# Optimization experiments

Measured on AMD Instinct MI355X. Metric: run time of the kernel, lower is better.

The kernel has to match this reference:

```python
import jax, jax.numpy as jnp
import numpy as np

D = 64       # d_model (channel)
NHEAD = 8    # heads in nn.MultiheadAttention
PROTO = 16   # proto_size == num_queries
EPS = 1e-5


def _haar_filters():
    L = np.array([1.0, 1.0], np.float32) / np.float32(np.sqrt(2.0))
    H = np.array([-1.0, 1.0], np.float32) / np.float32(np.sqrt(2.0))
    # WavePool: LL, LH, HL, HH Haar filters (2x2, stride 2, depthwise)
    return [jnp.asarray(np.outer(a, b)) for (a, b) in ((L, L), (L, H), (H, L), (H, H))]


def _dw(x, k2d, stride):
    # depthwise conv with the SAME 2D filter per channel; x: [B,C,H,W]
    C = x.shape[1]
    k = jnp.tile(k2d[None, None], (C, 1, 1, 1)).astype(x.dtype)
    return jax.lax.conv_general_dilated(x, k, (stride, stride), 'VALID',
        dimension_numbers=('NCHW', 'OIHW', 'NCHW'), feature_group_count=C)


def _ln(x, g, b):
    m = jnp.mean(x, -1, keepdims=True)
    v = jnp.var(x, -1, keepdims=True)
    return (x - m) * jax.lax.rsqrt(v + EPS) * g + b


def _bn(x, g, b, m, v):
    # eval-mode BatchNorm2d, x: [B,C,H,W]
    sh = (1, -1, 1, 1)
    return (x - m.reshape(sh)) * jax.lax.rsqrt(v.reshape(sh) + EPS) * g.reshape(sh) + b.reshape(sh)


def _mscw(x, lw1, lb1, lw2, lb2, gw1, gb1, gw2, gb2):
    pool = jnp.mean(x, axis=1, keepdims=True)            # [B,1,C]
    loc = jax.nn.relu(x @ lw1.T + lb1) @ lw2.T + lb2
    glo = jax.nn.relu(pool @ gw1.T + gb1) @ gw2.T + gb2
    return jax.nn.sigmoid(loc + glo)


def _mha(q, k, v, w_in, b_in, w_out, b_out):
    # standard nn.MultiheadAttention (batch_first), q:[B,Nq,D], k/v:[B,Nk,D]
    B, Nq, d = q.shape
    dk = d // NHEAD
    qp = q @ w_in[:d].T + b_in[:d]
    kp = k @ w_in[d:2 * d].T + b_in[d:2 * d]
    vp = v @ w_in[2 * d:].T + b_in[2 * d:]
    split = lambda t: t.reshape(t.shape[0], t.shape[1], NHEAD, dk).transpose(0, 2, 1, 3)
    qh, kh, vh = split(qp), split(kp), split(vp)
    scores = jnp.einsum('bhqd,bhkd->bhqk', qh, kh) * (1.0 / np.sqrt(dk))
    attn = jax.nn.softmax(scores, axis=-1)
    o = jnp.einsum('bhqk,bhkd->bhqd', attn, vh).transpose(0, 2, 1, 3).reshape(B, Nq, d)
    return o @ w_out.T + b_out


def reference(tgt, memory, pos, query_pos,
              w_in, b_in, w_out, b_out,
              ln1_g, ln1_b, ln2_g, ln2_b,
              m1_lw1, m1_lb1, m1_lw2, m1_lb2, m1_gw1, m1_gb1, m1_gw2, m1_gb2,
              m2_lw1, m2_lb1, m2_lw2, m2_lb2, m2_gw1, m2_gb1, m2_gw2, m2_gb2,
              dw_w, bn1_g, bn1_b, bn1_m, bn1_v, pw_w, bn2_g, bn2_b, bn2_m, bn2_v,
              mheads_w):
    # CrossAttentionLayer.forward_post -> custom MultiheadAttention.forward
    query = (tgt + query_pos).transpose(1, 0, 2)   # [B,Nq,C]
    key = (memory + pos).transpose(1, 0, 2)        # [B,N1,C]
    value = memory.transpose(1, 0, 2)
    B, N1, C = value.shape
    hw = int(np.sqrt(N1))
    feat = key.transpose(0, 2, 1).reshape(B, C, hw, hw)
    fLL, fLH, fHL, fHH = _haar_filters()
    LL = _dw(feat, fLL, 2)
    LH = _dw(feat, fLH, 2)
    HL = _dw(feat, fHL, 2)
    HH = _dw(feat, fHH, 2)
    high = (HL + LH + HH).reshape(B, C, -1).transpose(0, 2, 1)  # [B,N1/4,C]
    low = LL.reshape(B, C, -1).transpose(0, 2, 1)
    wei = _mscw(high + low, m1_lw1, m1_lb1, m1_lw2, m1_lb2, m1_gw1, m1_gb1, m1_gw2, m1_gb2)
    fre = wei * high + low
    x1 = _mha(query, fre, fre, w_in, b_in, w_out, b_out)
    x1 = _ln(x1 + query, ln1_g, ln1_b)
    # DSConv3x3: depthwise 3x3 + BN + ReLU, then 1x1 + BN + ReLU
    y = jax.lax.conv_general_dilated(feat, dw_w, (1, 1), ((1, 1), (1, 1)),
        dimension_numbers=('NCHW', 'OIHW', 'NCHW'), feature_group_count=C)
    y = jax.nn.relu(_bn(y, bn1_g, bn1_b, bn1_m, bn1_v))
    y = jax.lax.conv_general_dilated(y, pw_w, (1, 1), 'VALID',
        dimension_numbers=('NCHW', 'OIHW', 'NCHW'))
    y = jax.nn.relu(_bn(y, bn2_g, bn2_b, bn2_m, bn2_v))
    featf = y.reshape(B, C, -1).transpose(0, 2, 1)          # [B,N1,C]
    mw = jax.nn.softmax(featf @ mheads_w.T, axis=1)          # softmax over tokens, [B,N1,P]
    protos = jnp.einsum('bnp,bnc->bpc', mw, key)             # [B,P,C]
    attn2 = _mscw(protos + query, m2_lw1, m2_lb1, m2_lw2, m2_lb2, m2_gw1, m2_gb1, m2_gw2, m2_gb2)
    x2 = _ln(query * attn2 + query, ln2_g, ln2_b)
    return (x1 + x2).transpose(1, 0, 2)                      # [Nq,B,C]


def setup_inputs() -> dict:
    key = jax.random.key(0)
    ks = iter(jax.random.split(key, 40))
    B, HW, NQ = 8, 128, PROTO
    N1 = HW * HW
    wn = lambda *s: jax.random.normal(next(ks), s, jnp.float32) * 0.05
    inp = {
        'tgt': jax.random.normal(next(ks), (NQ, B, D), jnp.float32),
        'memory': jax.random.normal(next(ks), (N1, B, D), jnp.float32),
        'pos': jax.random.normal(next(ks), (N1, B, D), jnp.float32),
        'query_pos': jax.random.normal(next(ks), (NQ, B, D), jnp.float32),
        'w_in': wn(3 * D, D), 'b_in': jnp.zeros((3 * D,), jnp.float32),
        'w_out': wn(D, D), 'b_out': jnp.zeros((D,), jnp.float32),
        'ln1_g': jnp.ones((D,), jnp.float32), 'ln1_b': jnp.zeros((D,), jnp.float32),
        'ln2_g': jnp.ones((D,), jnp.float32), 'ln2_b': jnp.zeros((D,), jnp.float32),
        'dw_w': wn(D, 1, 3, 3),
        'bn1_g': jnp.ones((D,), jnp.float32), 'bn1_b': jnp.zeros((D,), jnp.float32),
        'bn1_m': jnp.zeros((D,), jnp.float32), 'bn1_v': jnp.ones((D,), jnp.float32),
        'pw_w': wn(D, D, 1, 1),
        'bn2_g': jnp.ones((D,), jnp.float32), 'bn2_b': jnp.zeros((D,), jnp.float32),
        'bn2_m': jnp.zeros((D,), jnp.float32), 'bn2_v': jnp.ones((D,), jnp.float32),
        'mheads_w': wn(PROTO, D),
    }
    for pfx in ('m1', 'm2'):
        for br in ('l', 'g'):
            inp[f'{pfx}_{br}w1'] = wn(D, D)
            inp[f'{pfx}_{br}b1'] = jnp.zeros((D,), jnp.float32)
            inp[f'{pfx}_{br}w2'] = wn(D, D)
            inp[f'{pfx}_{br}b2'] = jnp.zeros((D,), jnp.float32)
    return inp
```

## Files before the change

kernel.cpp:

```cpp
#include <hip/hip_runtime.h>
#include <math.h>

#define N1 16384
#define N2 4096

#define OFF_KEY   0L
#define OFF_KPH   4194304L
#define OFF_VPH   5242880L
#define OFF_PEXP  6291456L
#define OFF_WB    7340032L
#define OFF_CST   7350784L
#define OFF_POOL  7351552L
#define OFF_PROT  7352064L
#define OFF_ZZ    7360256L
#define OFF_GLO   7360384L
#define OFF_QP    7360896L
#define OFF_QB    7369088L
#define OFF_PART  7377280L

typedef __attribute__((ext_vector_type(8))) short bf16x8;
typedef __attribute__((ext_vector_type(4))) float floatx4;

#define MFMA16(a, b, c) __builtin_amdgcn_mfma_f32_16x16x32_bf16(a, b, c, 0, 0, 0)

__device__ __forceinline__ unsigned short f2bf(float f) {
    union { float f; unsigned u; } v; v.f = f;
    unsigned r = v.u + 0x7fffu + ((v.u >> 16) & 1u);
    return (unsigned short)(r >> 16);
}
__device__ __forceinline__ float bf2f(unsigned short s) {
    union { unsigned u; float f; } v; v.u = ((unsigned)s) << 16;
    return v.f;
}
__device__ __forceinline__ float sigmoidf_(float x) { return 1.f / (1.f + __expf(-x)); }
__device__ __forceinline__ bf16x8 ldg8b(const unsigned short* p) { return *(const bf16x8*)p; }
__device__ __forceinline__ void unpack8(uint4 v, float* f) {
    f[0] = bf2f((unsigned short)(v.x & 0xffff)); f[1] = bf2f((unsigned short)(v.x >> 16));
    f[2] = bf2f((unsigned short)(v.y & 0xffff)); f[3] = bf2f((unsigned short)(v.y >> 16));
    f[4] = bf2f((unsigned short)(v.z & 0xffff)); f[5] = bf2f((unsigned short)(v.z >> 16));
    f[6] = bf2f((unsigned short)(v.w & 0xffff)); f[7] = bf2f((unsigned short)(v.w >> 16));
}

__global__ __launch_bounds__(256) void k_prep(const float* __restrict__ lw1,
                                              const float* __restrict__ lw2,
                                              const float* __restrict__ w_in,
                                              const float* __restrict__ pw,
                                              const float* __restrict__ mh,
                                              const float* __restrict__ dw_w,
                                              const float* __restrict__ bn1_g, const float* __restrict__ bn1_b,
                                              const float* __restrict__ bn1_m, const float* __restrict__ bn1_v,
                                              const float* __restrict__ bn2_g, const float* __restrict__ bn2_b,
                                              const float* __restrict__ bn2_m, const float* __restrict__ bn2_v,
                                              unsigned short* __restrict__ wb,
                                              float* __restrict__ cst) {
    int i = blockIdx.x * 256 + threadIdx.x;
    if (i < 21504) {
        float v;
        if (i < 4096) v = lw1[i];
        else if (i < 8192) v = lw2[i - 4096];
        else if (i < 16384) v = w_in[4096 + (i - 8192)];
        else if (i < 20480) v = pw[i - 16384];
        else v = mh[i - 20480];
        wb[i] = f2bf(v);
    } else if (i < 22272) {
        int j = i - 21504;
        if (j < 576) {
            int k = j >> 6, c = j & 63;
            float s1 = bn1_g[c] * rsqrtf(bn1_v[c] + 1e-5f);
            cst[j] = dw_w[c * 9 + k] * s1;
        } else if (j < 640) {
            int c = j - 576;
            float s1 = bn1_g[c] * rsqrtf(bn1_v[c] + 1e-5f);
            cst[j] = bn1_b[c] - bn1_m[c] * s1;
        } else if (j < 704) {
            int c = j - 640;
            cst[j] = bn2_g[c] * rsqrtf(bn2_v[c] + 1e-5f);
        } else {
            int c = j - 704;
            float s2 = bn2_g[c] * rsqrtf(bn2_v[c] + 1e-5f);
            cst[j] = bn2_b[c] - bn2_m[c] * s2;
        }
    }
}

__global__ __launch_bounds__(256) void k_key(const float* __restrict__ mem,
                                             const float* __restrict__ pos,
                                             unsigned short* __restrict__ key,
                                             float* __restrict__ pool1raw) {
    __shared__ float sh[16][64];
    int tid = threadIdx.x;
    int b = blockIdx.x >> 9;
    int n_base = (blockIdx.x & 511) * 32;
    int c8 = tid & 7, local_n = tid >> 3;
    int n = n_base + local_n;
    long s4 = ((long)n * 8 + b) * 16 + c8 * 2;
    float4 m0 = ((const float4*)mem)[s4], m1 = ((const float4*)mem)[s4 + 1];
    float4 p0 = ((const float4*)pos)[s4], p1 = ((const float4*)pos)[s4 + 1];
    float f[8];
    f[0] = m0.x + p0.x; f[1] = m0.y + p0.y; f[2] = m0.z + p0.z; f[3] = m0.w + p0.w;
    f[4] = m1.x + p1.x; f[5] = m1.y + p1.y; f[6] = m1.z + p1.z; f[7] = m1.w + p1.w;
    uint4 o;
    o.x = (unsigned)f2bf(f[0]) | ((unsigned)f2bf(f[1]) << 16);
    o.y = (unsigned)f2bf(f[2]) | ((unsigned)f2bf(f[3]) << 16);
    o.z = (unsigned)f2bf(f[4]) | ((unsigned)f2bf(f[5]) << 16);
    o.w = (unsigned)f2bf(f[6]) | ((unsigned)f2bf(f[7]) << 16);
    ((uint4*)key)[(long)(b * 16384 + n) * 8 + c8] = o;
    int parity = (n_base >> 7) & 1;
    if (parity) {
        if (local_n & 1) {
            #pragma unroll
            for (int j = 0; j < 8; j++) sh[local_n >> 1][c8 * 8 + j] = f[j];
        }
        __syncthreads();
        if (tid < 64) {
            float s = 0.f;
            #pragma unroll
            for (int k = 0; k < 16; k++) s += sh[k][tid];
            atomicAdd(pool1raw + b * 64 + tid, s);
        }
    }
}

__global__ __launch_bounds__(64) void k_qp_glo(const float* __restrict__ tgt,
                                               const float* __restrict__ qpos,
                                               const float* __restrict__ w_in,
                                               const float* __restrict__ b_in,
                                               const float* __restrict__ pool1raw,
                                               const float* __restrict__ gw1, const float* __restrict__ gb1,
                                               const float* __restrict__ gw2, const float* __restrict__ gb2,
                                               float* __restrict__ qp,
                                               float* __restrict__ queryb,
                                               float* __restrict__ glo1) {
    __shared__ float s0[64], s1v[64];
    int t = threadIdx.x;
    if (blockIdx.x < 128) {
        int b = blockIdx.x >> 4;
        int q = blockIdx.x & 15;
        long src = ((long)q * 8 + b) * 64 + t;
        float v = tgt[src] + qpos[src];
        s0[t] = v;
        queryb[(b * 16 + q) * 64 + t] = v;
        __syncthreads();
        float acc = b_in[t];
        for (int c = 0; c < 64; c++) acc += s0[c] * w_in[t * 64 + c];
        qp[(b * 16 + q) * 64 + t] = acc;
    } else {
        int b = blockIdx.x - 128;
        s0[t] = pool1raw[b * 64 + t] * (2.0f / 4096.0f);
        __syncthreads();
        float h = gb1[t];
        for (int c = 0; c < 64; c++) h += s0[c] * gw1[t * 64 + c];
        s1v[t] = fmaxf(h, 0.f);
        __syncthreads();
        float gl = gb2[t];
        for (int hh = 0; hh < 64; hh++) gl += s1v[hh] * gw2[t * 64 + hh];
        glo1[b * 64 + t] = gl;
    }
}

__global__ __launch_bounds__(256) void k_mscw1(
        const unsigned short* __restrict__ keyb, const float* __restrict__ glo1,
        const float* __restrict__ lb1, const float* __restrict__ lb2,
        const float* __restrict__ b_in, const unsigned short* __restrict__ wb,
        unsigned short* __restrict__ kph, unsigned short* __restrict__ vph) {
    __shared__ __align__(16) short stage[256 * 72];
    __shared__ __align__(16) short hbuf[64 * 72];
    __shared__ __align__(16) short wbuf[64 * 72];
    int tid = threadIdx.x;
    int w = tid >> 6, l = tid & 63;
    int b = blockIdx.x >> 6, tile = blockIdx.x & 63;
    int m0 = w * 16, trow = l & 15, oct = l >> 4;
    const unsigned short* src = keyb + ((long)b * 16384 + tile * 256) * 64;
    #pragma unroll
    for (int k = 0; k < 8; k++) {
        int u = k * 256 + tid;
        int p = u >> 3, o = u & 7;
        uint4 v = *(const uint4*)(src + (long)u * 8);
        *(uint4*)(stage + p * 72 + o * 8) = v;
    }
    __syncthreads();
    int j = m0 + trow;
    float x[16], S[16];
    bf16x8 ax[2];
    #pragma unroll
    for (int half = 0; half < 2; half++) {
        int o = oct + half * 4;
        uint4 fa4 = *(const uint4*)(stage + (2 * j) * 72 + o * 8);
        uint4 fb4 = *(const uint4*)(stage + (2 * j + 1) * 72 + o * 8);
        uint4 fc4 = *(const uint4*)(stage + (128 + 2 * j) * 72 + o * 8);
        uint4 fd4 = *(const uint4*)(stage + (129 + 2 * j) * 72 + o * 8);
        float A[8], B[8], C[8], D[8];
        unpack8(fa4, A); unpack8(fb4, B); unpack8(fc4, C); unpack8(fd4, D);
        #pragma unroll
        for (int jj = 0; jj < 8; jj++) {
            float xd = 2.f * D[jj];
            x[half * 8 + jj] = xd;
            S[half * 8 + jj] = 0.5f * (A[jj] + B[jj] + C[jj] + D[jj]);
            ax[half][jj] = (short)f2bf(xd);
        }
    }
    const unsigned short* w1b = wb;
    const unsigned short* w2b = wb + 4096;
    const unsigned short* wkb = wb + 8192;
    const unsigned short* wvb = wb + 12288;
    #pragma unroll
    for (int t4 = 0; t4 < 4; t4++) {
        int n = t4 * 16 + trow;
        float bias = lb1[n];
        floatx4 acc = {bias, bias, bias, bias};
        acc = MFMA16(ax[0], ldg8b(w1b + n * 64 + oct * 8), acc);
        acc = MFMA16(ax[1], ldg8b(w1b + n * 64 + 32 + oct * 8), acc);
        #pragma unroll
        for (int r = 0; r < 4; r++)
            hbuf[(m0 + oct * 4 + r) * 72 + n] = (short)f2bf(fmaxf(acc[r], 0.f));
    }
    __syncthreads();
    {
        bf16x8 ah0 = *(const bf16x8*)(hbuf + (m0 + trow) * 72 + oct * 8);
        bf16x8 ah1 = *(const bf16x8*)(hbuf + (m0 + trow) * 72 + 32 + oct * 8);
        const float* gl = glo1 + b * 64;
        #pragma unroll
        for (int t4 = 0; t4 < 4; t4++) {
            int n = t4 * 16 + trow;
            float bias = lb2[n];
            floatx4 acc = {bias, bias, bias, bias};
            acc = MFMA16(ah0, ldg8b(w2b + n * 64 + oct * 8), acc);
            acc = MFMA16(ah1, ldg8b(w2b + n * 64 + 32 + oct * 8), acc);
            float g = gl[n];
            #pragma unroll
            for (int r = 0; r < 4; r++)
                wbuf[(m0 + oct * 4 + r) * 72 + n] = (short)f2bf(sigmoidf_(acc[r] + g));
        }
    }
    __syncthreads();
    bf16x8 af0, af1;
    {
        bf16x8 w0 = *(const bf16x8*)(wbuf + (m0 + trow) * 72 + oct * 8);
        bf16x8 w1v = *(const bf16x8*)(wbuf + (m0 + trow) * 72 + 32 + oct * 8);
        #pragma unroll
        for (int jj = 0; jj < 8; jj++) {
            float we0 = bf2f((unsigned short)w0[jj]);
            float we1 = bf2f((unsigned short)w1v[jj]);
            af0[jj] = (short)f2bf(we0 * x[jj] + (1.f - we0) * S[jj]);
            af1[jj] = (short)f2bf(we1 * x[8 + jj] + (1.f - we1) * S[8 + jj]);
        }
    }
    __syncthreads();
    short* kbuf = hbuf; short* vbuf = wbuf;
    #pragma unroll
    for (int t4 = 0; t4 < 4; t4++) {
        int ko = t4 * 16 + trow;
        float bk = b_in[64 + ko], bv = b_in[128 + ko];
        floatx4 ak = {bk, bk, bk, bk};
        floatx4 av = {bv, bv, bv, bv};
        ak = MFMA16(af0, ldg8b(wkb + ko * 64 + oct * 8), ak);
        ak = MFMA16(af1, ldg8b(wkb + ko * 64 + 32 + oct * 8), ak);
        av = MFMA16(af0, ldg8b(wvb + ko * 64 + oct * 8), av);
        av = MFMA16(af1, ldg8b(wvb + ko * 64 + 32 + oct * 8), av);
        #pragma unroll
        for (int r = 0; r < 4; r++) {
            int row = m0 + oct * 4 + r;
            kbuf[row * 72 + ko] = (short)f2bf(ak[r]);
            vbuf[row * 72 + ko] = (short)f2bf(av[r]);
        }
    }
    __syncthreads();
    for (int u = tid; u < 512; u += 256) {
        int h = u >> 6, tok = u & 63;
        uint4 kk = *(const uint4*)(kbuf + tok * 72 + h * 8);
        uint4 vv = *(const uint4*)(vbuf + tok * 72 + h * 8);
        long du = (long)(b * 8 + h) * 4096 + tile * 64 + tok;
        ((uint4*)kph)[du] = kk;
        ((uint4*)vph)[du] = vv;
    }
}

__global__ __launch_bounds__(512) void k_dsconv(
        const unsigned short* __restrict__ keyb,
        const unsigned short* __restrict__ wb,
        const float* __restrict__ cst,
        unsigned short* __restrict__ pexp, float* __restrict__ Z) {
    __shared__ __align__(16) short stage[3 * 128 * 72];
    __shared__ __align__(16) short pbuf[16 * 136];
    __shared__ float cbuf[768];
    __shared__ float zred[8][16];
    int tid = threadIdx.x;
    int w = tid >> 6, l = tid & 63;
    int b = blockIdx.x >> 7, h = blockIdx.x & 127;
    int p0 = w * 16, pr = l & 15, oct = l >> 4;
    for (int k = tid; k < 768; k += 512) cbuf[k] = cst[k];
    const unsigned short* kb = keyb + (long)b * 1048576;
    #pragma unroll
    for (int r = 0; r < 3; r++) {
        int row = h - 1 + r;
        if ((unsigned)row < 128u) {
            const unsigned short* src = kb + (long)row * 8192;
            #pragma unroll
            for (int k = 0; k < 4; k++) {
                int u = k * 512 + tid;
                int p = u >> 3, o = u & 7;
                uint4 v = *(const uint4*)(src + (long)u * 8);
                *(uint4*)(stage + (r * 128 + p) * 72 + o * 8) = v;
            }
        } else {
            uint4 zz = {0u, 0u, 0u, 0u};
            #pragma unroll
            for (int k = 0; k < 4; k++) {
                int u = k * 512 + tid;
                int p = u >> 3, o = u & 7;
                *(uint4*)(stage + (r * 128 + p) * 72 + o * 8) = zz;
            }
        }
    }
    __syncthreads();
    float accf[2][8];
    #pragma unroll
    for (int half = 0; half < 2; half++)
        #pragma unroll
        for (int jj = 0; jj < 8; jj++) accf[half][jj] = 0.f;
    #pragma unroll
    for (int r = 0; r < 3; r++) {
        #pragma unroll
        for (int kk = 0; kk < 3; kk++) {
            int col = p0 + pr - 1 + kk;
            if ((unsigned)col < 128u) {
                #pragma unroll
                for (int half = 0; half < 2; half++) {
                    int o = oct + half * 4;
                    uint4 d4 = *(const uint4*)(stage + (r * 128 + col) * 72 + o * 8);
                    float f[8]; unpack8(d4, f);
                    float4 wa = *(const float4*)(cbuf + (r * 3 + kk) * 64 + o * 8);
                    float4 wc = *(const float4*)(cbuf + (r * 3 + kk) * 64 + o * 8 + 4);
                    accf[half][0] += f[0] * wa.x; accf[half][1] += f[1] * wa.y;
                    accf[half][2] += f[2] * wa.z; accf[half][3] += f[3] * wa.w;
                    accf[half][4] += f[4] * wc.x; accf[half][5] += f[5] * wc.y;
                    accf[half][6] += f[6] * wc.z; accf[half][7] += f[7] * wc.w;
                }
            }
        }
    }
    bf16x8 af[2];
    #pragma unroll
    for (int half = 0; half < 2; half++) {
        int o = oct + half * 4;
        float4 oa = *(const float4*)(cbuf + 576 + o * 8);
        float4 ob = *(const float4*)(cbuf + 576 + o * 8 + 4);
        af[half][0] = (short)f2bf(fmaxf(accf[half][0] + oa.x, 0.f));
        af[half][1] = (short)f2bf(fmaxf(accf[half][1] + oa.y, 0.f));
        af[half][2] = (short)f2bf(fmaxf(accf[half][2] + oa.z, 0.f));
        af[half][3] = (short)f2bf(fmaxf(accf[half][3] + oa.w, 0.f));
        af[half][4] = (short)f2bf(fmaxf(accf[half][4] + ob.x, 0.f));
        af[half][5] = (short)f2bf(fmaxf(accf[half][5] + ob.y, 0.f));
        af[half][6] = (short)f2bf(fmaxf(accf[half][6] + ob.z, 0.f));
        af[half][7] = (short)f2bf(fmaxf(accf[half][7] + ob.w, 0.f));
    }
    __syncthreads();
    short* y2buf = stage;
    const unsigned short* pwb = wb + 16384;
    #pragma unroll
    for (int t4 = 0; t4 < 4; t4++) {
        int n = t4 * 16 + pr;
        floatx4 acc = {0.f, 0.f, 0.f, 0.f};
        acc = MFMA16(af[0], ldg8b(pwb + n * 64 + oct * 8), acc);
        acc = MFMA16(af[1], ldg8b(pwb + n * 64 + 32 + oct * 8), acc);
        float s2 = cbuf[640 + n], o2 = cbuf[704 + n];
        #pragma unroll
        for (int r = 0; r < 4; r++)
            y2buf[(p0 + oct * 4 + r) * 72 + n] = (short)f2bf(fmaxf(acc[r] * s2 + o2, 0.f));
    }
    __syncthreads();
    {
        const unsigned short* mhb = wb + 20480;
        bf16x8 a0 = *(const bf16x8*)(y2buf + (p0 + pr) * 72 + oct * 8);
        bf16x8 a1 = *(const bf16x8*)(y2buf + (p0 + pr) * 72 + 32 + oct * 8);
        floatx4 lg = {0.f, 0.f, 0.f, 0.f};
        lg = MFMA16(a0, ldg8b(mhb + pr * 64 + oct * 8), lg);
        lg = MFMA16(a1, ldg8b(mhb + pr * 64 + 32 + oct * 8), lg);
        float zs = 0.f;
        #pragma unroll
        for (int r = 0; r < 4; r++) {
            float e = __expf(lg[r]);
            zs += e;
            pbuf[pr * 136 + p0 + oct * 4 + r] = (short)f2bf(e);
        }
        zs += __shfl_xor(zs, 16);
        zs += __shfl_xor(zs, 32);
        if (l < 16) zred[w][l] = zs;
    }
    __syncthreads();
    if (tid < 256) {
        int p = tid >> 4, ch = tid & 15;
        uint4 o = *(const uint4*)(pbuf + p * 136 + ch * 8);
        ((uint4*)pexp)[((long)(b * 16 + p) * 16384 + h * 128 + ch * 8) >> 3] = o;
    }
    if (tid < 16) {
        float zt = 0.f;
        #pragma unroll
        for (int ww = 0; ww < 8; ww++) zt += zred[ww][tid];
        atomicAdd(Z + b * 16 + tid, zt);
    }
}

__global__ __launch_bounds__(256) void k_protos(const unsigned short* __restrict__ pexp,
                                                const unsigned short* __restrict__ keyb,
                                                float* __restrict__ protos) {
    __shared__ __align__(16) short ldsT[64 * 264];
    int tid = threadIdx.x;
    int b = blockIdx.x >> 6, ch = blockIdx.x & 63;
    long nbase = (long)b * 16384 + ch * 256;
    #pragma unroll
    for (int k = 0; k < 8; k++) {
        int u = k * 256 + tid;
        int n = u >> 3, o = u & 7;
        uint4 v = *(const uint4*)(keyb + (nbase + n) * 64 + o * 8);
        ldsT[(o * 8 + 0) * 264 + n] = (short)(v.x & 0xffff);
        ldsT[(o * 8 + 1) * 264 + n] = (short)(v.x >> 16);
        ldsT[(o * 8 + 2) * 264 + n] = (short)(v.y & 0xffff);
        ldsT[(o * 8 + 3) * 264 + n] = (short)(v.y >> 16);
        ldsT[(o * 8 + 4) * 264 + n] = (short)(v.z & 0xffff);
        ldsT[(o * 8 + 5) * 264 + n] = (short)(v.z >> 16);
        ldsT[(o * 8 + 6) * 264 + n] = (short)(v.w & 0xffff);
        ldsT[(o * 8 + 7) * 264 + n] = (short)(v.w >> 16);
    }
    __syncthreads();
    int w = tid >> 6, l = tid & 63;
    int col = l & 15, oct = l >> 4;
    const unsigned short* pb = pexp + ((long)b * 16 + col) * 16384 + ch * 256;
    floatx4 acc = {0.f, 0.f, 0.f, 0.f};
    #pragma unroll
    for (int s = 0; s < 8; s++) {
        bf16x8 A = *(const bf16x8*)(pb + s * 32 + oct * 8);
        bf16x8 B = *(const bf16x8*)(ldsT + (w * 16 + col) * 264 + s * 32 + oct * 8);
        acc = MFMA16(A, B, acc);
    }
    #pragma unroll
    for (int r = 0; r < 4; r++)
        atomicAdd(protos + (b * 16 + oct * 4 + r) * 64 + w * 16 + col, acc[r]);
}

__global__ __launch_bounds__(256) void k_mha(const float* __restrict__ qp,
                                             const unsigned short* __restrict__ kph,
                                             const unsigned short* __restrict__ vph,
                                             float* __restrict__ part) {
    int bh = blockIdx.x >> 3, seg = blockIdx.x & 7;
    int b = bh >> 3, hh = bh & 7;
    int tid = threadIdx.x;
    int q = tid >> 4, sub = tid & 15;
    const float* qv = qp + (long)(b * 16 + q) * 64 + hh * 8;
    float4 q0 = ((const float4*)qv)[0];
    float4 q1 = ((const float4*)qv)[1];
    const uint4* K4 = (const uint4*)kph + (long)bh * 4096;
    const uint4* V4 = (const uint4*)vph + (long)bh * 4096;
    const float scale = 0.35355339059327373f;
    float m = -1e30f, lsum = 0.f;
    float acc[8];
    #pragma unroll
    for (int d = 0; d < 8; d++) acc[d] = 0.f;
    for (int i = 0; i < 32; i++) {
        int n = seg * 512 + i * 16 + sub;
        float k8[8]; unpack8(K4[n], k8);
        float s = q0.x * k8[0] + q0.y * k8[1] + q0.z * k8[2] + q0.w * k8[3]
                + q1.x * k8[4] + q1.y * k8[5] + q1.z * k8[6] + q1.w * k8[7];
        s *= scale;
        float nm = fmaxf(m, s);
        float corr = __expf(m - nm);
        float wgt = __expf(s - nm);
        lsum = lsum * corr + wgt;
        float v8[8]; unpack8(V4[n], v8);
        #pragma unroll
        for (int d = 0; d < 8; d++) acc[d] = acc[d] * corr + wgt * v8[d];
        m = nm;
    }
    #pragma unroll
    for (int off = 1; off < 16; off <<= 1) {
        float om = __shfl_xor(m, off);
        float ol = __shfl_xor(lsum, off);
        float oa[8];
        #pragma unroll
        for (int d = 0; d < 8; d++) oa[d] = __shfl_xor(acc[d], off);
        float nm = fmaxf(m, om);
        float c1 = __expf(m - nm), c2 = __expf(om - nm);
        lsum = lsum * c1 + ol * c2;
        #pragma unroll
        for (int d = 0; d < 8; d++) acc[d] = acc[d] * c1 + oa[d] * c2;
        m = nm;
    }
    if (sub == 0) {
        float* P = part + ((long)(bh * 16 + q) * 8 + seg) * 12;
        P[0] = m; P[1] = lsum;
        #pragma unroll
        for (int d = 0; d < 8; d++) P[2 + d] = acc[d];
    }
}

__global__ __launch_bounds__(1024) void k_final(
        const float* __restrict__ queryb, const float* __restrict__ protos,
        const float* __restrict__ Z, const float* __restrict__ part,
        const float* __restrict__ w_out, const float* __restrict__ b_out,
        const float* __restrict__ ln1_g, const float* __restrict__ ln1_b,
        const float* __restrict__ ln2_g, const float* __restrict__ ln2_b,
        const float* __restrict__ lw1, const float* __restrict__ lb1,
        const float* __restrict__ lw2, const float* __restrict__ lb2,
        const float* __restrict__ gw1, const float* __restrict__ gb1,
        const float* __restrict__ gw2, const float* __restrict__ gb2,
        float* __restrict__ out) {
    int b = blockIdx.x;
    int t = threadIdx.x >> 6;
    int c = threadIdx.x & 63;
    __shared__ float xs[16][64], hid[16][64], os[16][64];
    __shared__ float pool[64], hidg[64], glo[64];
    float q = queryb[(long)(b * 16 + t) * 64 + c];
    float rz = 1.f / Z[b * 16 + t];
    float xin = protos[(long)(b * 16 + t) * 64 + c] * rz + q;
    xs[t][c] = xin;
    {
        int hh = c >> 3, d = c & 7;
        const float* P = part + ((long)((b * 8 + hh) * 16 + t) * 8) * 12;
        float mm = -1e30f, ll = 0.f, aa = 0.f;
        #pragma unroll
        for (int s = 0; s < 8; s++) {
            float pm = P[s * 12], pl2 = P[s * 12 + 1], pa = P[s * 12 + 2 + d];
            float nm = fmaxf(mm, pm);
            float c1 = __expf(mm - nm), c2 = __expf(pm - nm);
            aa = aa * c1 + pa * c2;
            ll = ll * c1 + pl2 * c2;
            mm = nm;
        }
        os[t][c] = aa / ll;
    }
    __syncthreads();
    if (threadIdx.x < 64) {
        float s = 0.f;
        for (int tt = 0; tt < 16; tt++) s += xs[tt][threadIdx.x];
        pool[threadIdx.x] = s * (1.f / 16.f);
    }
    __syncthreads();
    if (threadIdx.x < 64) {
        int hh = threadIdx.x;
        float a = gb1[hh];
        for (int cc = 0; cc < 64; cc++) a += pool[cc] * gw1[hh * 64 + cc];
        hidg[hh] = fmaxf(a, 0.f);
    }
    __syncthreads();
    if (threadIdx.x < 64) {
        int ccc = threadIdx.x;
        float a = gb2[ccc];
        for (int hh = 0; hh < 64; hh++) a += hidg[hh] * gw2[ccc * 64 + hh];
        glo[ccc] = a;
    }
    float a = lb1[c];
    for (int cc = 0; cc < 64; cc++) a += xs[t][cc] * lw1[c * 64 + cc];
    hid[t][c] = fmaxf(a, 0.f);
    __syncthreads();
    float loc = lb2[c];
    for (int hh = 0; hh < 64; hh++) loc += hid[t][hh] * lw2[c * 64 + hh];
    float attn2 = sigmoidf_(loc + glo[c]);
    float x2p = q * attn2 + q;
    float mu = x2p;
    for (int off = 32; off; off >>= 1) mu += __shfl_down(mu, off);
    mu = __shfl(mu, 0) * (1.f / 64.f);
    float d0 = x2p - mu;
    float vv = d0 * d0;
    for (int off = 32; off; off >>= 1) vv += __shfl_down(vv, off);
    vv = __shfl(vv, 0) * (1.f / 64.f);
    float x2 = d0 * rsqrtf(vv + 1e-5f) * ln2_g[c] + ln2_b[c];
    float x1p = b_out[c];
    for (int k = 0; k < 64; k++) x1p += os[t][k] * w_out[c * 64 + k];
    x1p += q;
    float mu1 = x1p;
    for (int off = 32; off; off >>= 1) mu1 += __shfl_down(mu1, off);
    mu1 = __shfl(mu1, 0) * (1.f / 64.f);
    float d1 = x1p - mu1;
    float v1 = d1 * d1;
    for (int off = 32; off; off >>= 1) v1 += __shfl_down(v1, off);
    v1 = __shfl(v1, 0) * (1.f / 64.f);
    float x1 = d1 * rsqrtf(v1 + 1e-5f) * ln1_g[c] + ln1_b[c];
    out[((long)t * 8 + b) * 64 + c] = x1 + x2;
}

extern "C" void kernel_launch(void* const* d_in, const int* in_sizes, int n_in,
                              void* d_out, int out_size, void* d_ws, size_t ws_size,
                              hipStream_t stream) {
    const float* tgt       = (const float*)d_in[0];
    const float* memory    = (const float*)d_in[1];
    const float* pos       = (const float*)d_in[2];
    const float* query_pos = (const float*)d_in[3];
    const float* w_in      = (const float*)d_in[4];
    const float* b_in      = (const float*)d_in[5];
    const float* w_out     = (const float*)d_in[6];
    const float* b_out     = (const float*)d_in[7];
    const float* ln1_g     = (const float*)d_in[8];
    const float* ln1_b     = (const float*)d_in[9];
    const float* ln2_g     = (const float*)d_in[10];
    const float* ln2_b     = (const float*)d_in[11];
    const float* dw_w      = (const float*)d_in[12];
    const float* bn1_g     = (const float*)d_in[13];
    const float* bn1_b     = (const float*)d_in[14];
    const float* bn1_m     = (const float*)d_in[15];
    const float* bn1_v     = (const float*)d_in[16];
    const float* pw_w      = (const float*)d_in[17];
    const float* bn2_g     = (const float*)d_in[18];
    const float* bn2_b     = (const float*)d_in[19];
    const float* bn2_m     = (const float*)d_in[20];
    const float* bn2_v     = (const float*)d_in[21];
    const float* mheads    = (const float*)d_in[22];
    const float* m1_lw1 = (const float*)d_in[23];
    const float* m1_lb1 = (const float*)d_in[24];
    const float* m1_lw2 = (const float*)d_in[25];
    const float* m1_lb2 = (const float*)d_in[26];
    const float* m1_gw1 = (const float*)d_in[27];
    const float* m1_gb1 = (const float*)d_in[28];
    const float* m1_gw2 = (const float*)d_in[29];
    const float* m1_gb2 = (const float*)d_in[30];
    const float* m2_lw1 = (const float*)d_in[31];
    const float* m2_lb1 = (const float*)d_in[32];
    const float* m2_lw2 = (const float*)d_in[33];
    const float* m2_lb2 = (const float*)d_in[34];
    const float* m2_gw1 = (const float*)d_in[35];
    const float* m2_gb1 = (const float*)d_in[36];
    const float* m2_gw2 = (const float*)d_in[37];
    const float* m2_gb2 = (const float*)d_in[38];

    float* ws = (float*)d_ws;
    float* out = (float*)d_out;
    unsigned short* keyb = (unsigned short*)(ws + OFF_KEY);
    unsigned short* kph  = (unsigned short*)(ws + OFF_KPH);
    unsigned short* vph  = (unsigned short*)(ws + OFF_VPH);
    unsigned short* pexp = (unsigned short*)(ws + OFF_PEXP);
    unsigned short* wb   = (unsigned short*)(ws + OFF_WB);

    hipMemsetAsync(ws + OFF_POOL, 0, 8832 * sizeof(float), stream);

    k_prep<<<88, 256, 0, stream>>>(m1_lw1, m1_lw2, w_in, pw_w, mheads, dw_w,
                                   bn1_g, bn1_b, bn1_m, bn1_v,
                                   bn2_g, bn2_b, bn2_m, bn2_v,
                                   wb, ws + OFF_CST);
    k_key<<<4096, 256, 0, stream>>>(memory, pos, keyb, ws + OFF_POOL);
    k_qp_glo<<<136, 64, 0, stream>>>(tgt, query_pos, w_in, b_in, ws + OFF_POOL,
                                     m1_gw1, m1_gb1, m1_gw2, m1_gb2,
                                     ws + OFF_QP, ws + OFF_QB, ws + OFF_GLO);
    k_mscw1<<<512, 256, 0, stream>>>(keyb, ws + OFF_GLO, m1_lb1, m1_lb2, b_in, wb, kph, vph);
    k_dsconv<<<1024, 512, 0, stream>>>(keyb, wb, ws + OFF_CST, pexp, ws + OFF_ZZ);
    k_protos<<<512, 256, 0, stream>>>(pexp, keyb, ws + OFF_PROT);
    k_mha<<<512, 256, 0, stream>>>(ws + OFF_QP, kph, vph, ws + OFF_PART);
    k_final<<<8, 1024, 0, stream>>>(ws + OFF_QB, ws + OFF_PROT, ws + OFF_ZZ, ws + OFF_PART,
                                    w_out, b_out, ln1_g, ln1_b, ln2_g, ln2_b,
                                    m2_lw1, m2_lb1, m2_lw2, m2_lb2,
                                    m2_gw1, m2_gb1, m2_gw2, m2_gb2,
                                    out);
}
```

Baseline: 267.4 us.

## Fuse prototype GEMM into dsconv, fold query projection into prep, drop pexp buffer

The prototype-weighted key reduction moves into k_dsconv. Each block now transposes its key tile in LDS and runs an MFMA against the softmax buffer, then adds the result into protos atomically. This removes the large bf16 pexp intermediate buffer and the separate k_protos kernel, and with them a write and re-read of several MB. The query projection moves into k_prep and the global-branch MLP is recomputed per block inside k_mscw1, which removes the k_qp_glo launch. Small weight matrices are pre-transposed in k_prep so the per-thread loops in k_final read coalesced memory. The cost is redundant global-MLP work in every k_mscw1 block and more atomic traffic from k_dsconv.

Result: faster. 247.7 us (-7.3%).

```diff
diff --git a/kernel.cpp b/kernel.cpp
--- a/kernel.cpp
+++ b/kernel.cpp
@@ -7,16 +7,14 @@
 #define OFF_KEY   0L
 #define OFF_KPH   4194304L
 #define OFF_VPH   5242880L
-#define OFF_PEXP  6291456L
-#define OFF_WB    7340032L
-#define OFF_CST   7350784L
-#define OFF_POOL  7351552L
-#define OFF_PROT  7352064L
-#define OFF_ZZ    7360256L
-#define OFF_GLO   7360384L
-#define OFF_QP    7360896L
-#define OFF_QB    7369088L
-#define OFF_PART  7377280L
+#define OFF_WB    6291456L
+#define OFF_CST   6302208L
+#define OFF_POOL  6331648L
+#define OFF_PROT  6332160L
+#define OFF_ZZ    6340352L
+#define OFF_QP    6340480L
+#define OFF_QB    6348672L
+#define OFF_PART  6356864L
 
 typedef __attribute__((ext_vector_type(8))) short bf16x8;
 typedef __attribute__((ext_vector_type(4))) float floatx4;
@@ -41,8 +39,8 @@
     f[6] = bf2f((unsigned short)(v.w & 0xffff)); f[7] = bf2f((unsigned short)(v.w >> 16));
 }
 
-__global__ __launch_bounds__(256) void k_prep(const float* __restrict__ lw1,
-                                              const float* __restrict__ lw2,
+__global__ __launch_bounds__(256) void k_prep(const float* __restrict__ m1lw1,
+                                              const float* __restrict__ m1lw2,
                                               const float* __restrict__ w_in,
                                               const float* __restrict__ pw,
                                               const float* __restrict__ mh,
@@ -51,35 +49,73 @@
                                               const float* __restrict__ bn1_m, const float* __restrict__ bn1_v,
                                               const float* __restrict__ bn2_g, const float* __restrict__ bn2_b,
                                               const float* __restrict__ bn2_m, const float* __restrict__ bn2_v,
+                                              const float* __restrict__ m1gw1, const float* __restrict__ m1gw2,
+                                              const float* __restrict__ m2gw1, const float* __restrict__ m2gw2,
+                                              const float* __restrict__ m2lw1, const float* __restrict__ m2lw2,
+                                              const float* __restrict__ w_out,
+                                              const float* __restrict__ tgt, const float* __restrict__ qpos,
+                                              const float* __restrict__ b_in,
                                               unsigned short* __restrict__ wb,
-                                              float* __restrict__ cst) {
-    int i = blockIdx.x * 256 + threadIdx.x;
-    if (i < 21504) {
+                                              float* __restrict__ cst,
+                                              float* __restrict__ qp, float* __restrict__ queryb) {
+    int blk = blockIdx.x, tid = threadIdx.x;
+    if (blk < 84) {
+        int i = blk * 256 + tid;
         float v;
-        if (i < 4096) v = lw1[i];
-        else if (i < 8192) v = lw2[i - 4096];
+        if (i < 4096) v = m1lw1[i];
+        else if (i < 8192) v = m1lw2[i - 4096];
         else if (i < 16384) v = w_in[4096 + (i - 8192)];
         else if (i < 20480) v = pw[i - 16384];
         else v = mh[i - 20480];
         wb[i] = f2bf(v);
-    } else if (i < 22272) {
-        int j = i - 21504;
+    } else if (blk < 199) {
+        int j = (blk - 84) * 256 + tid;
+        float v;
         if (j < 576) {
             int k = j >> 6, c = j & 63;
             float s1 = bn1_g[c] * rsqrtf(bn1_v[c] + 1e-5f);
-            cst[j] = dw_w[c * 9 + k] * s1;
+            v = dw_w[c * 9 + k] * s1;
         } else if (j < 640) {
             int c = j - 576;
             float s1 = bn1_g[c] * rsqrtf(bn1_v[c] + 1e-5f);
-            cst[j] = bn1_b[c] - bn1_m[c] * s1;
+            v = bn1_b[c] - bn1_m[c] * s1;
         } else if (j < 704) {
             int c = j - 640;
-            cst[j] = bn2_g[c] * rsqrtf(bn2_v[c] + 1e-5f);
-        } else {
+            v = bn2_g[c] * rsqrtf(bn2_v[c] + 1e-5f);
+        } else if (j < 768) {
             int c = j - 704;
             float s2 = bn2_g[c] * rsqrtf(bn2_v[c] + 1e-5f);
-            cst[j] = bn2_b[c] - bn2_m[c] * s2;
-        }
+            v = bn2_b[c] - bn2_m[c] * s2;
+        } else {
+            int jj = j - 768;
+            int m = jj >> 12, idx = jj & 4095;
+            int sidx = (idx & 63) * 64 + (idx >> 6);
+            const float* src;
+            switch (m) {
+                case 0: src = m1gw1; break;
+                case 1: src = m1gw2; break;
+                case 2: src = m2gw1; break;
+                case 3: src = m2gw2; break;
+                case 4: src = m2lw1; break;
+                case 5: src = m2lw2; break;
+                default: src = w_out; break;
+            }
+            v = src[sidx];
+        }
+        cst[j] = v;
+    } else {
+        __shared__ float qv[4][64];
+        int g = tid >> 6, lane = tid & 63;
+        int u = (blk - 199) * 4 + g;
+        int b = u >> 4, q = u & 15;
+        long src = ((long)q * 8 + b) * 64 + lane;
+        float v = tgt[src] + qpos[src];
+        qv[g][lane] = v;
+        queryb[(b * 16 + q) * 64 + lane] = v;
+        __syncthreads();
+        float acc = b_in[lane];
+        for (int cc = 0; cc < 64; cc++) acc += qv[g][cc] * w_in[lane * 64 + cc];
+        qp[(b * 16 + q) * 64 + lane] = acc;
     }
 }
 
@@ -121,55 +157,24 @@
     }
 }
 
-__global__ __launch_bounds__(64) void k_qp_glo(const float* __restrict__ tgt,
-                                               const float* __restrict__ qpos,
-                                               const float* __restrict__ w_in,
-                                               const float* __restrict__ b_in,
-                                               const float* __restrict__ pool1raw,
-                                               const float* __restrict__ gw1, const float* __restrict__ gb1,
-                                               const float* __restrict__ gw2, const float* __restrict__ gb2,
-                                               float* __restrict__ qp,
-                                               float* __restrict__ queryb,
-                                               float* __restrict__ glo1) {
-    __shared__ float s0[64], s1v[64];
-    int t = threadIdx.x;
-    if (blockIdx.x < 128) {
-        int b = blockIdx.x >> 4;
-        int q = blockIdx.x & 15;
-        long src = ((long)q * 8 + b) * 64 + t;
-        float v = tgt[src] + qpos[src];
-        s0[t] = v;
-        queryb[(b * 16 + q) * 64 + t] = v;
-        __syncthreads();
-        float acc = b_in[t];
-        for (int c = 0; c < 64; c++) acc += s0[c] * w_in[t * 64 + c];
-        qp[(b * 16 + q) * 64 + t] = acc;
-    } else {
-        int b = blockIdx.x - 128;
-        s0[t] = pool1raw[b * 64 + t] * (2.0f / 4096.0f);
-        __syncthreads();
-        float h = gb1[t];
-        for (int c = 0; c < 64; c++) h += s0[c] * gw1[t * 64 + c];
-        s1v[t] = fmaxf(h, 0.f);
-        __syncthreads();
-        float gl = gb2[t];
-        for (int hh = 0; hh < 64; hh++) gl += s1v[hh] * gw2[t * 64 + hh];
-        glo1[b * 64 + t] = gl;
-    }
-}
-
 __global__ __launch_bounds__(256) void k_mscw1(
-        const unsigned short* __restrict__ keyb, const float* __restrict__ glo1,
+        const unsigned short* __restrict__ keyb, const float* __restrict__ pool1raw,
         const float* __restrict__ lb1, const float* __restrict__ lb2,
+        const float* __restrict__ gb1, const float* __restrict__ gb2,
         const float* __restrict__ b_in, const unsigned short* __restrict__ wb,
+        const float* __restrict__ cst,
         unsigned short* __restrict__ kph, unsigned short* __restrict__ vph) {
     __shared__ __align__(16) short stage[256 * 72];
     __shared__ __align__(16) short hbuf[64 * 72];
     __shared__ __align__(16) short wbuf[64 * 72];
+    __shared__ float parr[64], gtmp[64], gbuf[64];
     int tid = threadIdx.x;
     int w = tid >> 6, l = tid & 63;
     int b = blockIdx.x >> 6, tile = blockIdx.x & 63;
     int m0 = w * 16, trow = l & 15, oct = l >> 4;
+    const float* gw1T = cst + 768;
+    const float* gw2T = cst + 4864;
+    if (tid < 64) parr[tid] = pool1raw[b * 64 + tid] * (2.0f / 4096.0f);
     const unsigned short* src = keyb + ((long)b * 16384 + tile * 256) * 64;
     #pragma unroll
     for (int k = 0; k < 8; k++) {
@@ -179,6 +184,11 @@
         *(uint4*)(stage + p * 72 + o * 8) = v;
     }
     __syncthreads();
+    if (tid < 64) {
+        float a = gb1[tid];
+        for (int cc = 0; cc < 64; cc++) a += parr[cc] * gw1T[cc * 64 + tid];
+        gtmp[tid] = fmaxf(a, 0.f);
+    }
     int j = m0 + trow;
     float x[16], S[16];
     bf16x8 ax[2];
@@ -215,10 +225,15 @@
             hbuf[(m0 + oct * 4 + r) * 72 + n] = (short)f2bf(fmaxf(acc[r], 0.f));
     }
     __syncthreads();
+    if (tid < 64) {
+        float g = gb2[tid];
+        for (int hh = 0; hh < 64; hh++) g += gtmp[hh] * gw2T[hh * 64 + tid];
+        gbuf[tid] = g;
+    }
+    __syncthreads();
     {
         bf16x8 ah0 = *(const bf16x8*)(hbuf + (m0 + trow) * 72 + oct * 8);
         bf16x8 ah1 = *(const bf16x8*)(hbuf + (m0 + trow) * 72 + 32 + oct * 8);
-        const float* gl = glo1 + b * 64;
         #pragma unroll
         for (int t4 = 0; t4 < 4; t4++) {
             int n = t4 * 16 + trow;
@@ -226,7 +241,7 @@
             floatx4 acc = {bias, bias, bias, bias};
             acc = MFMA16(ah0, ldg8b(w2b + n * 64 + oct * 8), acc);
             acc = MFMA16(ah1, ldg8b(w2b + n * 64 + 32 + oct * 8), acc);
-            float g = gl[n];
+            float g = gbuf[n];
             #pragma unroll
             for (int r = 0; r < 4; r++)
                 wbuf[(m0 + oct * 4 + r) * 72 + n] = (short)f2bf(sigmoidf_(acc[r] + g));
@@ -279,7 +294,7 @@
         const unsigned short* __restrict__ keyb,
         const unsigned short* __restrict__ wb,
         const float* __restrict__ cst,
-        unsigned short* __restrict__ pexp, float* __restrict__ Z) {
+        float* __restrict__ protos, float* __restrict__ Z) {
     __shared__ __align__(16) short stage[3 * 128 * 72];
     __shared__ __align__(16) short pbuf[16 * 136];
     __shared__ float cbuf[768];
@@ -356,17 +371,35 @@
     }
     __syncthreads();
     short* y2buf = stage;
-    const unsigned short* pwb = wb + 16384;
-    #pragma unroll
-    for (int t4 = 0; t4 < 4; t4++) {
-        int n = t4 * 16 + pr;
-        floatx4 acc = {0.f, 0.f, 0.f, 0.f};
-        acc = MFMA16(af[0], ldg8b(pwb + n * 64 + oct * 8), acc);
-        acc = MFMA16(af[1], ldg8b(pwb + n * 64 + 32 + oct * 8), acc);
-        float s2 = cbuf[640 + n], o2 = cbuf[704 + n];
-        #pragma unroll
-        for (int r = 0; r < 4; r++)
-            y2buf[(p0 + oct * 4 + r) * 72 + n] = (short)f2bf(fmaxf(acc[r] * s2 + o2, 0.f));
+    short* KT = stage + 18432;
+    {
+        const unsigned short* pwb = wb + 16384;
+        #pragma unroll
+        for (int t4 = 0; t4 < 4; t4++) {
+            int n = t4 * 16 + pr;
+            floatx4 acc = {0.f, 0.f, 0.f, 0.f};
+            acc = MFMA16(af[0], ldg8b(pwb + n * 64 + oct * 8), acc);
+            acc = MFMA16(af[1], ldg8b(pwb + n * 64 + 32 + oct * 8), acc);
+            float s2 = cbuf[640 + n], o2 = cbuf[704 + n];
+            #pragma unroll
+            for (int r = 0; r < 4; r++)
+                y2buf[(p0 + oct * 4 + r) * 72 + n] = (short)f2bf(fmaxf(acc[r] * s2 + o2, 0.f));
+        }
+        #pragma unroll
+        for (int k = 0; k < 2; k++) {
+            int u = k * 512 + tid;
+            int n = u >> 3, o = u & 7;
+            uint4 v = *(const uint4*)(stage + (128 + n) * 72 + o * 8);
+            int nx = n ^ (o << 3);
+            KT[(o * 8 + 0) * 136 + nx] = (short)(v.x & 0xffff);
+            KT[(o * 8 + 1) * 136 + nx] = (short)(v.x >> 16);
+            KT[(o * 8 + 2) * 136 + nx] = (short)(v.y & 0xffff);
+            KT[(o * 8 + 3) * 136 + nx] = (short)(v.y >> 16);
+            KT[(o * 8 + 4) * 136 + nx] = (short)(v.z & 0xffff);
+            KT[(o * 8 + 5) * 136 + nx] = (short)(v.z >> 16);
+            KT[(o * 8 + 6) * 136 + nx] = (short)(v.w & 0xffff);
+            KT[(o * 8 + 7) * 136 + nx] = (short)(v.w >> 16);
+        }
     }
     __syncthreads();
     {
@@ -388,10 +421,20 @@
         if (l < 16) zred[w][l] = zs;
     }
     __syncthreads();
-    if (tid < 256) {
-        int p = tid >> 4, ch = tid & 15;
-        uint4 o = *(const uint4*)(pbuf + p * 136 + ch * 8);
-        ((uint4*)pexp)[((long)(b * 16 + p) * 16384 + h * 128 + ch * 8) >> 3] = o;
+    if (w < 4) {
+        int ct = w;
+        int c = ct * 16 + pr;
+        int xrc = ((c >> 3) & 7) << 3;
+        floatx4 acc = {0.f, 0.f, 0.f, 0.f};
+        #pragma unroll
+        for (int s = 0; s < 4; s++) {
+            bf16x8 A = *(const bf16x8*)(pbuf + pr * 136 + s * 32 + oct * 8);
+            bf16x8 B = *(const bf16x8*)(KT + c * 136 + ((s * 32 + oct * 8) ^ xrc));
+            acc = MFMA16(A, B, acc);
+        }
+        #pragma unroll
+        for (int r = 0; r < 4; r++)
+            atomicAdd(protos + (b * 16 + oct * 4 + r) * 64 + c, acc[r]);
     }
     if (tid < 16) {
         float zt = 0.f;
@@ -399,43 +442,6 @@
         for (int ww = 0; ww < 8; ww++) zt += zred[ww][tid];
         atomicAdd(Z + b * 16 + tid, zt);
     }
-}
-
-__global__ __launch_bounds__(256) void k_protos(const unsigned short* __restrict__ pexp,
-                                                const unsigned short* __restrict__ keyb,
-                                                float* __restrict__ protos) {
-    __shared__ __align__(16) short ldsT[64 * 264];
-    int tid = threadIdx.x;
-    int b = blockIdx.x >> 6, ch = blockIdx.x & 63;
-    long nbase = (long)b * 16384 + ch * 256;
-    #pragma unroll
-    for (int k = 0; k < 8; k++) {
-        int u = k * 256 + tid;
-        int n = u >> 3, o = u & 7;
-        uint4 v = *(const uint4*)(keyb + (nbase + n) * 64 + o * 8);
-        ldsT[(o * 8 + 0) * 264 + n] = (short)(v.x & 0xffff);
-        ldsT[(o * 8 + 1) * 264 + n] = (short)(v.x >> 16);
-        ldsT[(o * 8 + 2) * 264 + n] = (short)(v.y & 0xffff);
-        ldsT[(o * 8 + 3) * 264 + n] = (short)(v.y >> 16);
-        ldsT[(o * 8 + 4) * 264 + n] = (short)(v.z & 0xffff);
-        ldsT[(o * 8 + 5) * 264 + n] = (short)(v.z >> 16);
-        ldsT[(o * 8 + 6) * 264 + n] = (short)(v.w & 0xffff);
-        ldsT[(o * 8 + 7) * 264 + n] = (short)(v.w >> 16);
-    }
-    __syncthreads();
-    int w = tid >> 6, l = tid & 63;
-    int col = l & 15, oct = l >> 4;
-    const unsigned short* pb = pexp + ((long)b * 16 + col) * 16384 + ch * 256;
-    floatx4 acc = {0.f, 0.f, 0.f, 0.f};
-    #pragma unroll
-    for (int s = 0; s < 8; s++) {
-        bf16x8 A = *(const bf16x8*)(pb + s * 32 + oct * 8);
-        bf16x8 B = *(const bf16x8*)(ldsT + (w * 16 + col) * 264 + s * 32 + oct * 8);
-        acc = MFMA16(A, B, acc);
-    }
-    #pragma unroll
-    for (int r = 0; r < 4; r++)
-        atomicAdd(protos + (b * 16 + oct * 4 + r) * 64 + w * 16 + col, acc[r]);
 }
 
 __global__ __launch_bounds__(256) void k_mha(const float* __restrict__ qp,
@@ -496,14 +502,18 @@
 __global__ __launch_bounds__(1024) void k_final(
         const float* __restrict__ queryb, const float* __restrict__ protos,
         const float* __restrict__ Z, const float* __restrict__ part,
-        const float* __restrict__ w_out, const float* __restrict__ b_out,
+        const float* __restrict__ cst,
+        const float* __restrict__ b_out,
         const float* __restrict__ ln1_g, const float* __restrict__ ln1_b,
         const float* __restrict__ ln2_g, const float* __restrict__ ln2_b,
-        const float* __restrict__ lw1, const float* __restrict__ lb1,
-        const float* __restrict__ lw2, const float* __restrict__ lb2,
-        const float* __restrict__ gw1, const float* __restrict__ gb1,
-        const float* __restrict__ gw2, const float* __restrict__ gb2,
+        const float* __restrict__ lb1, const float* __restrict__ lb2,
+        const float* __restrict__ gb1, const float* __restrict__ gb2,
         float* __restrict__ out) {
+    const float* gw1T = cst + 8960;
+    const float* gw2T = cst + 13056;
+    const float* lw1T = cst + 17152;
+    const float* lw2T = cst + 21248;
+    const float* woT  = cst + 25344;
     int b = blockIdx.x;
     int t = threadIdx.x >> 6;
     int c = threadIdx.x & 63;
@@ -538,22 +548,22 @@
     if (threadIdx.x < 64) {
         int hh = threadIdx.x;
         float a = gb1[hh];
-        for (int cc = 0; cc < 64; cc++) a += pool[cc] * gw1[hh * 64 + cc];
+        for (int cc = 0; cc < 64; cc++) a += pool[cc] * gw1T[cc * 64 + hh];
         hidg[hh] = fmaxf(a, 0.f);
     }
     __syncthreads();
     if (threadIdx.x < 64) {
         int ccc = threadIdx.x;
         float a = gb2[ccc];
-        for (int hh = 0; hh < 64; hh++) a += hidg[hh] * gw2[ccc * 64 + hh];
+        for (int hh = 0; hh < 64; hh++) a += hidg[hh] * gw2T[hh * 64 + ccc];
         glo[ccc] = a;
     }
     float a = lb1[c];
-    for (int cc = 0; cc < 64; cc++) a += xs[t][cc] * lw1[c * 64 + cc];
+    for (int cc = 0; cc < 64; cc++) a += xs[t][cc] * lw1T[cc * 64 + c];
     hid[t][c] = fmaxf(a, 0.f);
     __syncthreads();
     float loc = lb2[c];
-    for (int hh = 0; hh < 64; hh++) loc += hid[t][hh] * lw2[c * 64 + hh];
+    for (int hh = 0; hh < 64; hh++) loc += hid[t][hh] * lw2T[hh * 64 + c];
     float attn2 = sigmoidf_(loc + glo[c]);
     float x2p = q * attn2 + q;
     float mu = x2p;
@@ -565,7 +575,7 @@
     vv = __shfl(vv, 0) * (1.f / 64.f);
     float x2 = d0 * rsqrtf(vv + 1e-5f) * ln2_g[c] + ln2_b[c];
     float x1p = b_out[c];
-    for (int k = 0; k < 64; k++) x1p += os[t][k] * w_out[c * 64 + k];
+    for (int k = 0; k < 64; k++) x1p += os[t][k] * woT[k * 64 + c];
     x1p += q;
     float mu1 = x1p;
     for (int off = 32; off; off >>= 1) mu1 += __shfl_down(mu1, off);
@@ -626,26 +636,26 @@
     unsigned short* keyb = (unsigned short*)(ws + OFF_KEY);
     unsigned short* kph  = (unsigned short*)(ws + OFF_KPH);
     unsigned short* vph  = (unsigned short*)(ws + OFF_VPH);
-    unsigned short* pexp = (unsigned short*)(ws + OFF_PEXP);
     unsigned short* wb   = (unsigned short*)(ws + OFF_WB);
 
     hipMemsetAsync(ws + OFF_POOL, 0, 8832 * sizeof(float), stream);
 
-    k_prep<<<88, 256, 0, stream>>>(m1_lw1, m1_lw2, w_in, pw_w, mheads, dw_w,
-                                   bn1_g, bn1_b, bn1_m, bn1_v,
-                                   bn2_g, bn2_b, bn2_m, bn2_v,
-                                   wb, ws + OFF_CST);
+    k_prep<<<231, 256, 0, stream>>>(m1_lw1, m1_lw2, w_in, pw_w, mheads, dw_w,
+                                    bn1_g, bn1_b, bn1_m, bn1_v,
+                                    bn2_g, bn2_b, bn2_m, bn2_v,
+                                    m1_gw1, m1_gw2, m2_gw1, m2_gw2,
+                                    m2_lw1, m2_lw2, w_out,
+                                    tgt, query_pos, b_in,
+                                    wb, ws + OFF_CST, ws + OFF_QP, ws + OFF_QB);
     k_key<<<4096, 256, 0, stream>>>(memory, pos, keyb, ws + OFF_POOL);
-    k_qp_glo<<<136, 64, 0, stream>>>(tgt, query_pos, w_in, b_in, ws + OFF_POOL,
-                                     m1_gw1, m1_gb1, m1_gw2, m1_gb2,
-                                     ws + OFF_QP, ws + OFF_QB, ws + OFF_GLO);
-    k_mscw1<<<512, 256, 0, stream>>>(keyb, ws + OFF_GLO, m1_lb1, m1_lb2, b_in, wb, kph, vph);
-    k_dsconv<<<1024, 512, 0, stream>>>(keyb, wb, ws + OFF_CST, pexp, ws + OFF_ZZ);
-    k_protos<<<512, 256, 0, stream>>>(pexp, keyb, ws + OFF_PROT);
+    k_mscw1<<<512, 256, 0, stream>>>(keyb, ws + OFF_POOL, m1_lb1, m1_lb2,
+                                     m1_gb1, m1_gb2, b_in, wb, ws + OFF_CST, kph, vph);
+    k_dsconv<<<1024, 512, 0, stream>>>(keyb, wb, ws + OFF_CST,
+                                       ws + OFF_PROT, ws + OFF_ZZ);
     k_mha<<<512, 256, 0, stream>>>(ws + OFF_QP, kph, vph, ws + OFF_PART);
     k_final<<<8, 1024, 0, stream>>>(ws + OFF_QB, ws + OFF_PROT, ws + OFF_ZZ, ws + OFF_PART,
-                                    w_out, b_out, ln1_g, ln1_b, ln2_g, ln2_b,
-                                    m2_lw1, m2_lb1, m2_lw2, m2_lb2,
-                                    m2_gw1, m2_gb1, m2_gw2, m2_gb2,
+                                    ws + OFF_CST, b_out,
+                                    ln1_g, ln1_b, ln2_g, ln2_b,
+                                    m2_lb1, m2_lb2, m2_gb1, m2_gb2,
                                     out);
 }
```
